# Kernel tuning notes

Hardware: AMD Instinct MI355X
Metric: run time of the kernel (lower is better)

## Reference

```python
import jax, jax.numpy as jnp
import numpy as np

N_NODES = 500000
N_EDGES = 5000000
D = 16


def _glorot(key, shape):
    fan_in, fan_out = shape[1], shape[0]
    lim = (6.0 / (fan_in + fan_out)) ** 0.5
    return jax.random.uniform(key, shape, jnp.float32, -lim, lim)


def setup_inputs() -> dict:
    key = jax.random.key(0)
    ks = jax.random.split(key, 12)
    x = jax.random.normal(ks[0], (N_NODES, D), jnp.float32)
    edge_index = jax.random.randint(ks[1], (2, N_EDGES), 0, N_NODES, jnp.int32)
    # GraphConv params: lin_rel (weight+bias, applied to aggregated neighbors),
    # lin_root (weight only, applied to self features)
    conv1_w_rel = _glorot(ks[2], (D, D))
    conv1_b_rel = jnp.zeros((D,), jnp.float32)
    conv1_w_root = _glorot(ks[3], (D, D))
    conv2_w_rel = _glorot(ks[4], (D, D))
    conv2_b_rel = jnp.zeros((D,), jnp.float32)
    conv2_w_root = _glorot(ks[5], (D, D))
    fc1_w = _glorot(ks[6], (8, D))
    fc1_b = jnp.zeros((8,), jnp.float32)
    fc2_w = _glorot(ks[7], (2, 8))
    fc2_b = jnp.zeros((2,), jnp.float32)
    return {
        "x": x, "edge_index": edge_index,
        "conv1_w_rel": conv1_w_rel, "conv1_b_rel": conv1_b_rel, "conv1_w_root": conv1_w_root,
        "conv2_w_rel": conv2_w_rel, "conv2_b_rel": conv2_b_rel, "conv2_w_root": conv2_w_root,
        "fc1_w": fc1_w, "fc1_b": fc1_b, "fc2_w": fc2_w, "fc2_b": fc2_b,
    }


def graph_conv(x, edge_index, w_rel, b_rel, w_root):
    # PyG GraphConv (aggr='add'): out_i = W_rel @ sum_{j->i} x_j + b_rel + W_root @ x_i
    src, dst = edge_index[0], edge_index[1]
    msgs = x[src]  # [E, D] gather of source-node features
    agg = jax.ops.segment_sum(msgs, dst, num_segments=x.shape[0])  # [N, D]
    return agg @ w_rel.T + b_rel + x @ w_root.T


def reference(x, edge_index,
              conv1_w_rel, conv1_b_rel, conv1_w_root,
              conv2_w_rel, conv2_b_rel, conv2_w_root,
              fc1_w, fc1_b, fc2_w, fc2_b):
    h = jax.nn.relu(graph_conv(x, edge_index, conv1_w_rel, conv1_b_rel, conv1_w_root))
    h = jax.nn.relu(graph_conv(h, edge_index, conv2_w_rel, conv2_b_rel, conv2_w_root))
    h = jax.nn.relu(h @ fc1_w.T + fc1_b)
    return h @ fc2_w.T + fc2_b
```

## Files before the change

kernel.cpp:

```cpp
#include <hip/hip_runtime.h>

#define N_NODES 500000
#define N_EDGES 5000000
#define D 16

__global__ __launch_bounds__(256) void scatter_add_kernel(
    const float* __restrict__ feat,
    const int* __restrict__ edge_index,
    float* __restrict__ agg) {
    long tid = (long)blockIdx.x * blockDim.x + threadIdx.x;
    long total = (long)N_EDGES * D;
    if (tid >= total) return;
    int e = (int)(tid >> 4);
    int d = (int)(tid & 15);
    int s = edge_index[e];
    int t = edge_index[N_EDGES + e];
    float v = feat[(long)s * D + d];
    atomicAdd(&agg[(long)t * D + d], v);
}

__global__ __launch_bounds__(256) void node1_kernel(
    const float* __restrict__ x,
    const float* __restrict__ agg,
    const float* __restrict__ w_rel,
    const float* __restrict__ b_rel,
    const float* __restrict__ w_root,
    float* __restrict__ h) {
    __shared__ float sWrel[D * D];
    __shared__ float sWroot[D * D];
    __shared__ float sB[D];
    for (int i = threadIdx.x; i < D * D; i += blockDim.x) {
        sWrel[i] = w_rel[i];
        sWroot[i] = w_root[i];
    }
    if (threadIdx.x < D) sB[threadIdx.x] = b_rel[threadIdx.x];
    __syncthreads();

    int i = blockIdx.x * blockDim.x + threadIdx.x;
    if (i >= N_NODES) return;

    float a[D], xi[D];
    {
        const float4* ap = (const float4*)(agg + (long)i * D);
        const float4* xp = (const float4*)(x + (long)i * D);
        #pragma unroll
        for (int q = 0; q < 4; ++q) {
            float4 av = ap[q];
            float4 xv = xp[q];
            a[q * 4 + 0] = av.x; a[q * 4 + 1] = av.y; a[q * 4 + 2] = av.z; a[q * 4 + 3] = av.w;
            xi[q * 4 + 0] = xv.x; xi[q * 4 + 1] = xv.y; xi[q * 4 + 2] = xv.z; xi[q * 4 + 3] = xv.w;
        }
    }

    float4* hp = (float4*)(h + (long)i * D);
    #pragma unroll
    for (int q = 0; q < 4; ++q) {
        float4 o;
        float* op = &o.x;
        #pragma unroll
        for (int r = 0; r < 4; ++r) {
            int dd = q * 4 + r;
            float acc = sB[dd];
            #pragma unroll
            for (int k = 0; k < D; ++k)
                acc += a[k] * sWrel[dd * D + k] + xi[k] * sWroot[dd * D + k];
            op[r] = acc > 0.f ? acc : 0.f;
        }
        hp[q] = o;
    }
}

__global__ __launch_bounds__(256) void node2_kernel(
    const float* __restrict__ h1,
    const float* __restrict__ agg,
    const float* __restrict__ w_rel,
    const float* __restrict__ b_rel,
    const float* __restrict__ w_root,
    const float* __restrict__ fc1_w,
    const float* __restrict__ fc1_b,
    const float* __restrict__ fc2_w,
    const float* __restrict__ fc2_b,
    float* __restrict__ out) {
    __shared__ float sWrel[D * D];
    __shared__ float sWroot[D * D];
    __shared__ float sB[D];
    __shared__ float sF1w[8 * D];
    __shared__ float sF1b[8];
    __shared__ float sF2w[2 * 8];
    __shared__ float sF2b[2];
    for (int i = threadIdx.x; i < D * D; i += blockDim.x) {
        sWrel[i] = w_rel[i];
        sWroot[i] = w_root[i];
    }
    if (threadIdx.x < D) sB[threadIdx.x] = b_rel[threadIdx.x];
    if (threadIdx.x < 8 * D) sF1w[threadIdx.x] = fc1_w[threadIdx.x];
    if (threadIdx.x < 8) sF1b[threadIdx.x] = fc1_b[threadIdx.x];
    if (threadIdx.x < 16) sF2w[threadIdx.x] = fc2_w[threadIdx.x];
    if (threadIdx.x < 2) sF2b[threadIdx.x] = fc2_b[threadIdx.x];
    __syncthreads();

    int i = blockIdx.x * blockDim.x + threadIdx.x;
    if (i >= N_NODES) return;

    float a[D], xi[D];
    {
        const float4* ap = (const float4*)(agg + (long)i * D);
        const float4* xp = (const float4*)(h1 + (long)i * D);
        #pragma unroll
        for (int q = 0; q < 4; ++q) {
            float4 av = ap[q];
            float4 xv = xp[q];
            a[q * 4 + 0] = av.x; a[q * 4 + 1] = av.y; a[q * 4 + 2] = av.z; a[q * 4 + 3] = av.w;
            xi[q * 4 + 0] = xv.x; xi[q * 4 + 1] = xv.y; xi[q * 4 + 2] = xv.z; xi[q * 4 + 3] = xv.w;
        }
    }

    float h2[D];
    #pragma unroll
    for (int dd = 0; dd < D; ++dd) {
        float acc = sB[dd];
        #pragma unroll
        for (int k = 0; k < D; ++k)
            acc += a[k] * sWrel[dd * D + k] + xi[k] * sWroot[dd * D + k];
        h2[dd] = acc > 0.f ? acc : 0.f;
    }

    float h3[8];
    #pragma unroll
    for (int j = 0; j < 8; ++j) {
        float acc = sF1b[j];
        #pragma unroll
        for (int k = 0; k < D; ++k) acc += h2[k] * sF1w[j * D + k];
        h3[j] = acc > 0.f ? acc : 0.f;
    }

    float2 o;
    {
        float acc0 = sF2b[0], acc1 = sF2b[1];
        #pragma unroll
        for (int j = 0; j < 8; ++j) {
            acc0 += h3[j] * sF2w[0 * 8 + j];
            acc1 += h3[j] * sF2w[1 * 8 + j];
        }
        o.x = acc0;
        o.y = acc1;
    }
    ((float2*)out)[i] = o;
}

extern "C" void kernel_launch(void* const* d_in, const int* in_sizes, int n_in,
                              void* d_out, int out_size, void* d_ws, size_t ws_size,
                              hipStream_t stream) {
    const float* x          = (const float*)d_in[0];
    const int*   edge_index = (const int*)d_in[1];
    const float* c1_wrel    = (const float*)d_in[2];
    const float* c1_brel    = (const float*)d_in[3];
    const float* c1_wroot   = (const float*)d_in[4];
    const float* c2_wrel    = (const float*)d_in[5];
    const float* c2_brel    = (const float*)d_in[6];
    const float* c2_wroot   = (const float*)d_in[7];
    const float* fc1_w      = (const float*)d_in[8];
    const float* fc1_b      = (const float*)d_in[9];
    const float* fc2_w      = (const float*)d_in[10];
    const float* fc2_b      = (const float*)d_in[11];
    float* out = (float*)d_out;

    float* agg = (float*)d_ws;
    float* h1  = agg + (long)N_NODES * D;
    size_t feat_bytes = (size_t)N_NODES * D * sizeof(float);

    const int BLK = 256;
    long scatter_total = (long)N_EDGES * D;
    int scatter_blocks = (int)((scatter_total + BLK - 1) / BLK);
    int node_blocks = (N_NODES + BLK - 1) / BLK;

    hipMemsetAsync(agg, 0, feat_bytes, stream);
    scatter_add_kernel<<<scatter_blocks, BLK, 0, stream>>>(x, edge_index, agg);
    node1_kernel<<<node_blocks, BLK, 0, stream>>>(x, agg, c1_wrel, c1_brel, c1_wroot, h1);

    hipMemsetAsync(agg, 0, feat_bytes, stream);
    scatter_add_kernel<<<scatter_blocks, BLK, 0, stream>>>(h1, edge_index, agg);
    node2_kernel<<<node_blocks, BLK, 0, stream>>>(h1, agg, c2_wrel, c2_brel, c2_wroot,
                                                  fc1_w, fc1_b, fc2_w, fc2_b, out);
}
```

Before: 702.6 us.

## Build CSR by destination and replace atomic scatter with pull-based gather

Builds a CSR keyed by destination node on every call: degree histogram, a three-kernel prefix scan, then an atomic-cursor reorder of source indices. Both conv layers then pull neighbour features per node with 16 threads per node and fuse aggregation with the node linear layers, removing the 80M float atomics and the agg buffers with their memsets. The price is CSR construction each call, which costs 10M integer atomics plus extra launches, and per-node loops whose length depends on degree.

```diff
diff --git a/kernel.cpp b/kernel.cpp
--- a/kernel.cpp
+++ b/kernel.cpp
@@ -4,148 +4,196 @@
 #define N_EDGES 5000000
 #define D 16
 
-__global__ __launch_bounds__(256) void scatter_add_kernel(
-    const float* __restrict__ feat,
-    const int* __restrict__ edge_index,
-    float* __restrict__ agg) {
-    long tid = (long)blockIdx.x * blockDim.x + threadIdx.x;
-    long total = (long)N_EDGES * D;
-    if (tid >= total) return;
-    int e = (int)(tid >> 4);
-    int d = (int)(tid & 15);
+#define SCAN_CHUNK 1024
+#define NSCAN_BLOCKS ((N_NODES + SCAN_CHUNK - 1) / SCAN_CHUNK)
+
+__global__ __launch_bounds__(256) void hist_kernel(
+    const int* __restrict__ edge_index, int* __restrict__ deg) {
+    int e = blockIdx.x * 256 + threadIdx.x;
+    if (e < N_EDGES) atomicAdd(&deg[edge_index[N_EDGES + e]], 1);
+}
+
+__global__ __launch_bounds__(256) void scan_blocks_kernel(
+    const int* __restrict__ deg, int* __restrict__ scanned,
+    int* __restrict__ partials) {
+    __shared__ int sdata[256];
+    int t = threadIdx.x;
+    int base = blockIdx.x * SCAN_CHUNK + t * 4;
+    int v0 = 0, v1 = 0, v2 = 0, v3 = 0;
+    if (base + 0 < N_NODES) v0 = deg[base + 0];
+    if (base + 1 < N_NODES) v1 = deg[base + 1];
+    if (base + 2 < N_NODES) v2 = deg[base + 2];
+    if (base + 3 < N_NODES) v3 = deg[base + 3];
+    int tsum = v0 + v1 + v2 + v3;
+    sdata[t] = tsum;
+    __syncthreads();
+    for (int off = 1; off < 256; off <<= 1) {
+        int val = (t >= off) ? sdata[t - off] : 0;
+        __syncthreads();
+        if (t >= off) sdata[t] += val;
+        __syncthreads();
+    }
+    int excl = sdata[t] - tsum;
+    if (t == 255) partials[blockIdx.x] = sdata[255];
+    int p = excl;
+    if (base + 0 < N_NODES) scanned[base + 0] = p; p += v0;
+    if (base + 1 < N_NODES) scanned[base + 1] = p; p += v1;
+    if (base + 2 < N_NODES) scanned[base + 2] = p; p += v2;
+    if (base + 3 < N_NODES) scanned[base + 3] = p;
+}
+
+__global__ __launch_bounds__(512) void scan_partials_kernel(int* __restrict__ partials) {
+    __shared__ int sdata[512];
+    int t = threadIdx.x;
+    int v = (t < NSCAN_BLOCKS) ? partials[t] : 0;
+    sdata[t] = v;
+    __syncthreads();
+    for (int off = 1; off < 512; off <<= 1) {
+        int val = (t >= off) ? sdata[t - off] : 0;
+        __syncthreads();
+        if (t >= off) sdata[t] += val;
+        __syncthreads();
+    }
+    if (t < NSCAN_BLOCKS) partials[t] = sdata[t] - v;
+}
+
+__global__ __launch_bounds__(256) void scan_add_kernel(
+    const int* __restrict__ scanned, const int* __restrict__ partials,
+    int* __restrict__ rowptr, int* __restrict__ cursor) {
+    int i = blockIdx.x * 256 + threadIdx.x;
+    if (i < N_NODES) {
+        int v = scanned[i] + partials[i / SCAN_CHUNK];
+        rowptr[i] = v;
+        cursor[i] = v;
+    }
+    if (i == 0) rowptr[N_NODES] = N_EDGES;
+}
+
+__global__ __launch_bounds__(256) void reorder_kernel(
+    const int* __restrict__ edge_index, int* __restrict__ cursor,
+    int* __restrict__ csr_src) {
+    int e = blockIdx.x * 256 + threadIdx.x;
+    if (e >= N_EDGES) return;
     int s = edge_index[e];
     int t = edge_index[N_EDGES + e];
-    float v = feat[(long)s * D + d];
-    atomicAdd(&agg[(long)t * D + d], v);
-}
-
-__global__ __launch_bounds__(256) void node1_kernel(
+    int pos = atomicAdd(&cursor[t], 1);
+    csr_src[pos] = s;
+}
+
+__global__ __launch_bounds__(256) void gather_node1_kernel(
     const float* __restrict__ x,
-    const float* __restrict__ agg,
-    const float* __restrict__ w_rel,
-    const float* __restrict__ b_rel,
+    const int* __restrict__ rowptr, const int* __restrict__ csr_src,
+    const float* __restrict__ w_rel, const float* __restrict__ b_rel,
+    const float* __restrict__ w_root, float* __restrict__ h) {
+    __shared__ float sWrelT[D * D];
+    __shared__ float sWrootT[D * D];
+    __shared__ float sB[D];
+    __shared__ float sAgg[16][D + 1];
+    __shared__ float sX[16][D + 1];
+
+    {
+        int r = threadIdx.x >> 4, c = threadIdx.x & 15;
+        sWrelT[c * D + r] = w_rel[r * D + c];
+        sWrootT[c * D + r] = w_root[r * D + c];
+        if (threadIdx.x < D) sB[threadIdx.x] = b_rel[threadIdx.x];
+    }
+    __syncthreads();
+
+    int g = threadIdx.x >> 4;
+    int d = threadIdx.x & 15;
+    int node = blockIdx.x * 16 + g;
+
+    if (node < N_NODES) {
+        int r0 = rowptr[node], r1 = rowptr[node + 1];
+        float acc = 0.f;
+        for (int j = r0; j < r1; ++j) {
+            int s = csr_src[j];
+            acc += x[(long)s * D + d];
+        }
+        sAgg[g][d] = acc;
+        sX[g][d] = x[(long)node * D + d];
+    }
+    __syncthreads();
+
+    if (node < N_NODES) {
+        float accO = sB[d];
+        #pragma unroll
+        for (int k = 0; k < D; ++k)
+            accO += sAgg[g][k] * sWrelT[k * D + d] + sX[g][k] * sWrootT[k * D + d];
+        h[(long)node * D + d] = accO > 0.f ? accO : 0.f;
+    }
+}
+
+__global__ __launch_bounds__(256) void gather_node2_kernel(
+    const float* __restrict__ h1,
+    const int* __restrict__ rowptr, const int* __restrict__ csr_src,
+    const float* __restrict__ w_rel, const float* __restrict__ b_rel,
     const float* __restrict__ w_root,
-    float* __restrict__ h) {
-    __shared__ float sWrel[D * D];
-    __shared__ float sWroot[D * D];
-    __shared__ float sB[D];
-    for (int i = threadIdx.x; i < D * D; i += blockDim.x) {
-        sWrel[i] = w_rel[i];
-        sWroot[i] = w_root[i];
-    }
-    if (threadIdx.x < D) sB[threadIdx.x] = b_rel[threadIdx.x];
-    __syncthreads();
-
-    int i = blockIdx.x * blockDim.x + threadIdx.x;
-    if (i >= N_NODES) return;
-
-    float a[D], xi[D];
-    {
-        const float4* ap = (const float4*)(agg + (long)i * D);
-        const float4* xp = (const float4*)(x + (long)i * D);
-        #pragma unroll
-        for (int q = 0; q < 4; ++q) {
-            float4 av = ap[q];
-            float4 xv = xp[q];
-            a[q * 4 + 0] = av.x; a[q * 4 + 1] = av.y; a[q * 4 + 2] = av.z; a[q * 4 + 3] = av.w;
-            xi[q * 4 + 0] = xv.x; xi[q * 4 + 1] = xv.y; xi[q * 4 + 2] = xv.z; xi[q * 4 + 3] = xv.w;
-        }
-    }
-
-    float4* hp = (float4*)(h + (long)i * D);
-    #pragma unroll
-    for (int q = 0; q < 4; ++q) {
-        float4 o;
-        float* op = &o.x;
-        #pragma unroll
-        for (int r = 0; r < 4; ++r) {
-            int dd = q * 4 + r;
-            float acc = sB[dd];
-            #pragma unroll
-            for (int k = 0; k < D; ++k)
-                acc += a[k] * sWrel[dd * D + k] + xi[k] * sWroot[dd * D + k];
-            op[r] = acc > 0.f ? acc : 0.f;
-        }
-        hp[q] = o;
-    }
-}
-
-__global__ __launch_bounds__(256) void node2_kernel(
-    const float* __restrict__ h1,
-    const float* __restrict__ agg,
-    const float* __restrict__ w_rel,
-    const float* __restrict__ b_rel,
-    const float* __restrict__ w_root,
-    const float* __restrict__ fc1_w,
-    const float* __restrict__ fc1_b,
-    const float* __restrict__ fc2_w,
-    const float* __restrict__ fc2_b,
+    const float* __restrict__ fc1_w, const float* __restrict__ fc1_b,
+    const float* __restrict__ fc2_w, const float* __restrict__ fc2_b,
     float* __restrict__ out) {
-    __shared__ float sWrel[D * D];
-    __shared__ float sWroot[D * D];
+    __shared__ float sWrelT[D * D];
+    __shared__ float sWrootT[D * D];
     __shared__ float sB[D];
     __shared__ float sF1w[8 * D];
     __shared__ float sF1b[8];
     __shared__ float sF2w[2 * 8];
     __shared__ float sF2b[2];
-    for (int i = threadIdx.x; i < D * D; i += blockDim.x) {
-        sWrel[i] = w_rel[i];
-        sWroot[i] = w_root[i];
-    }
-    if (threadIdx.x < D) sB[threadIdx.x] = b_rel[threadIdx.x];
-    if (threadIdx.x < 8 * D) sF1w[threadIdx.x] = fc1_w[threadIdx.x];
-    if (threadIdx.x < 8) sF1b[threadIdx.x] = fc1_b[threadIdx.x];
-    if (threadIdx.x < 16) sF2w[threadIdx.x] = fc2_w[threadIdx.x];
-    if (threadIdx.x < 2) sF2b[threadIdx.x] = fc2_b[threadIdx.x];
-    __syncthreads();
-
-    int i = blockIdx.x * blockDim.x + threadIdx.x;
-    if (i >= N_NODES) return;
-
-    float a[D], xi[D];
+    __shared__ float sAgg[16][D + 1];
+    __shared__ float sX[16][D + 1];
+    __shared__ float sH2[16][D + 1];
+
     {
-        const float4* ap = (const float4*)(agg + (long)i * D);
-        const float4* xp = (const float4*)(h1 + (long)i * D);
-        #pragma unroll
-        for (int q = 0; q < 4; ++q) {
-            float4 av = ap[q];
-            float4 xv = xp[q];
-            a[q * 4 + 0] = av.x; a[q * 4 + 1] = av.y; a[q * 4 + 2] = av.z; a[q * 4 + 3] = av.w;
-            xi[q * 4 + 0] = xv.x; xi[q * 4 + 1] = xv.y; xi[q * 4 + 2] = xv.z; xi[q * 4 + 3] = xv.w;
+        int r = threadIdx.x >> 4, c = threadIdx.x & 15;
+        sWrelT[c * D + r] = w_rel[r * D + c];
+        sWrootT[c * D + r] = w_root[r * D + c];
+        if (threadIdx.x < D) sB[threadIdx.x] = b_rel[threadIdx.x];
+        if (threadIdx.x < 8 * D) sF1w[threadIdx.x] = fc1_w[threadIdx.x];
+        if (threadIdx.x < 8) sF1b[threadIdx.x] = fc1_b[threadIdx.x];
+        if (threadIdx.x < 16) sF2w[threadIdx.x] = fc2_w[threadIdx.x];
+        if (threadIdx.x < 2) sF2b[threadIdx.x] = fc2_b[threadIdx.x];
+    }
+    __syncthreads();
+
+    int g = threadIdx.x >> 4;
+    int d = threadIdx.x & 15;
+    int node = blockIdx.x * 16 + g;
+
+    if (node < N_NODES) {
+        int r0 = rowptr[node], r1 = rowptr[node + 1];
+        float acc = 0.f;
+        for (int j = r0; j < r1; ++j) {
+            int s = csr_src[j];
+            acc += h1[(long)s * D + d];
         }
-    }
-
-    float h2[D];
-    #pragma unroll
-    for (int dd = 0; dd < D; ++dd) {
-        float acc = sB[dd];
+        sAgg[g][d] = acc;
+        sX[g][d] = h1[(long)node * D + d];
+    }
+    __syncthreads();
+
+    if (node < N_NODES) {
+        float accO = sB[d];
         #pragma unroll
         for (int k = 0; k < D; ++k)
-            acc += a[k] * sWrel[dd * D + k] + xi[k] * sWroot[dd * D + k];
-        h2[dd] = acc > 0.f ? acc : 0.f;
-    }
-
-    float h3[8];
-    #pragma unroll
-    for (int j = 0; j < 8; ++j) {
-        float acc = sF1b[j];
-        #pragma unroll
-        for (int k = 0; k < D; ++k) acc += h2[k] * sF1w[j * D + k];
-        h3[j] = acc > 0.f ? acc : 0.f;
-    }
-
-    float2 o;
-    {
-        float acc0 = sF2b[0], acc1 = sF2b[1];
+            accO += sAgg[g][k] * sWrelT[k * D + d] + sX[g][k] * sWrootT[k * D + d];
+        sH2[g][d] = accO > 0.f ? accO : 0.f;
+    }
+    __syncthreads();
+
+    if (node < N_NODES && d < 2) {
+        float h3[8];
         #pragma unroll
         for (int j = 0; j < 8; ++j) {
-            acc0 += h3[j] * sF2w[0 * 8 + j];
-            acc1 += h3[j] * sF2w[1 * 8 + j];
+            float acc = sF1b[j];
+            #pragma unroll
+            for (int k = 0; k < D; ++k) acc += sH2[g][k] * sF1w[j * D + k];
+            h3[j] = acc > 0.f ? acc : 0.f;
         }
-        o.x = acc0;
-        o.y = acc1;
-    }
-    ((float2*)out)[i] = o;
+        float o = sF2b[d];
+        #pragma unroll
+        for (int j = 0; j < 8; ++j) o += h3[j] * sF2w[d * 8 + j];
+        out[(long)node * 2 + d] = o;
+    }
 }
 
 extern "C" void kernel_launch(void* const* d_in, const int* in_sizes, int n_in,
@@ -165,21 +213,30 @@
     const float* fc2_b      = (const float*)d_in[11];
     float* out = (float*)d_out;
 
-    float* agg = (float*)d_ws;
-    float* h1  = agg + (long)N_NODES * D;
-    size_t feat_bytes = (size_t)N_NODES * D * sizeof(float);
+    int* csr_src  = (int*)d_ws;
+    int* rowptr   = csr_src + N_EDGES;
+    int* cursor   = rowptr + (N_NODES + 1);
+    int* deg      = cursor + N_NODES;
+    int* scanned  = deg + N_NODES;
+    int* partials = scanned + N_NODES;
+    float* h1     = (float*)(partials + 512);
 
     const int BLK = 256;
-    long scatter_total = (long)N_EDGES * D;
-    int scatter_blocks = (int)((scatter_total + BLK - 1) / BLK);
-    int node_blocks = (N_NODES + BLK - 1) / BLK;
-
-    hipMemsetAsync(agg, 0, feat_bytes, stream);
-    scatter_add_kernel<<<scatter_blocks, BLK, 0, stream>>>(x, edge_index, agg);
-    node1_kernel<<<node_blocks, BLK, 0, stream>>>(x, agg, c1_wrel, c1_brel, c1_wroot, h1);
-
-    hipMemsetAsync(agg, 0, feat_bytes, stream);
-    scatter_add_kernel<<<scatter_blocks, BLK, 0, stream>>>(h1, edge_index, agg);
-    node2_kernel<<<node_blocks, BLK, 0, stream>>>(h1, agg, c2_wrel, c2_brel, c2_wroot,
-                                                  fc1_w, fc1_b, fc2_w, fc2_b, out);
-}
+    int edge_blocks = (N_EDGES + BLK - 1) / BLK;
+    int node_blocks16 = (N_NODES + 15) / 16;
+    int node_blocks256 = (N_NODES + BLK - 1) / BLK;
+
+    hipMemsetAsync(deg, 0, N_NODES * sizeof(int), stream);
+    hist_kernel<<<edge_blocks, BLK, 0, stream>>>(edge_index, deg);
+    scan_blocks_kernel<<<NSCAN_BLOCKS, BLK, 0, stream>>>(deg, scanned, partials);
+    scan_partials_kernel<<<1, 512, 0, stream>>>(partials);
+    scan_add_kernel<<<node_blocks256, BLK, 0, stream>>>(scanned, partials, rowptr, cursor);
+    reorder_kernel<<<edge_blocks, BLK, 0, stream>>>(edge_index, cursor, csr_src);
+
+    gather_node1_kernel<<<node_blocks16, BLK, 0, stream>>>(
+        x, rowptr, csr_src, c1_wrel, c1_brel, c1_wroot, h1);
+
+    gather_node2_kernel<<<node_blocks16, BLK, 0, stream>>>(
+        h1, rowptr, csr_src, c2_wrel, c2_brel, c2_wroot,
+        fc1_w, fc1_b, fc2_w, fc2_b, out);
+}
```

Measured after the change: 1.321 ms. 1.88x slower.

## Store aggregation and hidden features in fp16 with packed half2 atomics

Applied to the files above, without the earlier changes.

The aggregation buffer and the intermediate layer-1 features move from fp32 to packed half2. Each thread now handles two features, using one packed fp16 atomic add per pair, so the count of atomics and the bytes moved in the scatter-add halve. The node kernels convert between fp16 and fp32 at load and store time. The cost is reduced precision in summed neighbour aggregates, with rounding error in the accumulation and possible overflow for high-degree nodes.

```diff
diff --git a/kernel.cpp b/kernel.cpp
--- a/kernel.cpp
+++ b/kernel.cpp
@@ -1,31 +1,45 @@
 #include <hip/hip_runtime.h>
+#include <hip/hip_fp16.h>
 
 #define N_NODES 500000
 #define N_EDGES 5000000
 #define D 16
 
-__global__ __launch_bounds__(256) void scatter_add_kernel(
-    const float* __restrict__ feat,
+__global__ __launch_bounds__(256) void scatter1_kernel(
+    const float* __restrict__ x,
     const int* __restrict__ edge_index,
-    float* __restrict__ agg) {
-    long tid = (long)blockIdx.x * blockDim.x + threadIdx.x;
-    long total = (long)N_EDGES * D;
-    if (tid >= total) return;
-    int e = (int)(tid >> 4);
-    int d = (int)(tid & 15);
+    __half2* __restrict__ agg) {
+    long tid = (long)blockIdx.x * 256 + threadIdx.x;
+    if (tid >= (long)N_EDGES * 8) return;
+    int e = (int)(tid >> 3);
+    int p = (int)(tid & 7);
     int s = edge_index[e];
     int t = edge_index[N_EDGES + e];
-    float v = feat[(long)s * D + d];
-    atomicAdd(&agg[(long)t * D + d], v);
+    float2 v = ((const float2*)(x + (long)s * D))[p];
+    unsafeAtomicAdd(&agg[(long)t * 8 + p], __float22half2_rn(v));
+}
+
+__global__ __launch_bounds__(256) void scatter2_kernel(
+    const __half2* __restrict__ h1,
+    const int* __restrict__ edge_index,
+    __half2* __restrict__ agg) {
+    long tid = (long)blockIdx.x * 256 + threadIdx.x;
+    if (tid >= (long)N_EDGES * 8) return;
+    int e = (int)(tid >> 3);
+    int p = (int)(tid & 7);
+    int s = edge_index[e];
+    int t = edge_index[N_EDGES + e];
+    __half2 v = h1[(long)s * 8 + p];
+    unsafeAtomicAdd(&agg[(long)t * 8 + p], v);
 }
 
 __global__ __launch_bounds__(256) void node1_kernel(
     const float* __restrict__ x,
-    const float* __restrict__ agg,
+    const __half2* __restrict__ agg,
     const float* __restrict__ w_rel,
     const float* __restrict__ b_rel,
     const float* __restrict__ w_root,
-    float* __restrict__ h) {
+    __half2* __restrict__ h1) {
     __shared__ float sWrel[D * D];
     __shared__ float sWroot[D * D];
     __shared__ float sB[D];
@@ -41,38 +55,48 @@
 
     float a[D], xi[D];
     {
-        const float4* ap = (const float4*)(agg + (long)i * D);
+        __half2 hrow[8];
+        const float4* ap = (const float4*)(agg + (long)i * 8);
+        *(float4*)&hrow[0] = ap[0];
+        *(float4*)&hrow[4] = ap[1];
+        #pragma unroll
+        for (int q = 0; q < 8; ++q) {
+            float2 f = __half22float2(hrow[q]);
+            a[2 * q] = f.x; a[2 * q + 1] = f.y;
+        }
         const float4* xp = (const float4*)(x + (long)i * D);
         #pragma unroll
         for (int q = 0; q < 4; ++q) {
-            float4 av = ap[q];
             float4 xv = xp[q];
-            a[q * 4 + 0] = av.x; a[q * 4 + 1] = av.y; a[q * 4 + 2] = av.z; a[q * 4 + 3] = av.w;
-            xi[q * 4 + 0] = xv.x; xi[q * 4 + 1] = xv.y; xi[q * 4 + 2] = xv.z; xi[q * 4 + 3] = xv.w;
-        }
-    }
-
-    float4* hp = (float4*)(h + (long)i * D);
+            xi[q * 4 + 0] = xv.x; xi[q * 4 + 1] = xv.y;
+            xi[q * 4 + 2] = xv.z; xi[q * 4 + 3] = xv.w;
+        }
+    }
+
+    __half2 hout[8];
     #pragma unroll
-    for (int q = 0; q < 4; ++q) {
-        float4 o;
-        float* op = &o.x;
-        #pragma unroll
-        for (int r = 0; r < 4; ++r) {
-            int dd = q * 4 + r;
+    for (int q = 0; q < 8; ++q) {
+        float o0, o1;
+        #pragma unroll
+        for (int r = 0; r < 2; ++r) {
+            int dd = 2 * q + r;
             float acc = sB[dd];
             #pragma unroll
             for (int k = 0; k < D; ++k)
                 acc += a[k] * sWrel[dd * D + k] + xi[k] * sWroot[dd * D + k];
-            op[r] = acc > 0.f ? acc : 0.f;
-        }
-        hp[q] = o;
-    }
+            acc = acc > 0.f ? acc : 0.f;
+            if (r == 0) o0 = acc; else o1 = acc;
+        }
+        hout[q] = __float22half2_rn(make_float2(o0, o1));
+    }
+    float4* hp = (float4*)(h1 + (long)i * 8);
+    hp[0] = *(float4*)&hout[0];
+    hp[1] = *(float4*)&hout[4];
 }
 
 __global__ __launch_bounds__(256) void node2_kernel(
-    const float* __restrict__ h1,
-    const float* __restrict__ agg,
+    const __half2* __restrict__ h1,
+    const __half2* __restrict__ agg,
     const float* __restrict__ w_rel,
     const float* __restrict__ b_rel,
     const float* __restrict__ w_root,
@@ -104,14 +128,22 @@
 
     float a[D], xi[D];
     {
-        const float4* ap = (const float4*)(agg + (long)i * D);
-        const float4* xp = (const float4*)(h1 + (long)i * D);
-        #pragma unroll
-        for (int q = 0; q < 4; ++q) {
-            float4 av = ap[q];
-            float4 xv = xp[q];
-            a[q * 4 + 0] = av.x; a[q * 4 + 1] = av.y; a[q * 4 + 2] = av.z; a[q * 4 + 3] = av.w;
-            xi[q * 4 + 0] = xv.x; xi[q * 4 + 1] = xv.y; xi[q * 4 + 2] = xv.z; xi[q * 4 + 3] = xv.w;
+        __half2 hrow[8];
+        const float4* ap = (const float4*)(agg + (long)i * 8);
+        *(float4*)&hrow[0] = ap[0];
+        *(float4*)&hrow[4] = ap[1];
+        #pragma unroll
+        for (int q = 0; q < 8; ++q) {
+            float2 f = __half22float2(hrow[q]);
+            a[2 * q] = f.x; a[2 * q + 1] = f.y;
+        }
+        const float4* xp = (const float4*)(h1 + (long)i * 8);
+        *(float4*)&hrow[0] = xp[0];
+        *(float4*)&hrow[4] = xp[1];
+        #pragma unroll
+        for (int q = 0; q < 8; ++q) {
+            float2 f = __half22float2(hrow[q]);
+            xi[2 * q] = f.x; xi[2 * q + 1] = f.y;
         }
     }
 
@@ -165,21 +197,21 @@
     const float* fc2_b      = (const float*)d_in[11];
     float* out = (float*)d_out;
 
-    float* agg = (float*)d_ws;
-    float* h1  = agg + (long)N_NODES * D;
-    size_t feat_bytes = (size_t)N_NODES * D * sizeof(float);
+    __half2* agg = (__half2*)d_ws;
+    __half2* h1  = agg + (long)N_NODES * 8;
+    size_t agg_bytes = (size_t)N_NODES * 8 * sizeof(__half2);
 
     const int BLK = 256;
-    long scatter_total = (long)N_EDGES * D;
+    long scatter_total = (long)N_EDGES * 8;
     int scatter_blocks = (int)((scatter_total + BLK - 1) / BLK);
     int node_blocks = (N_NODES + BLK - 1) / BLK;
 
-    hipMemsetAsync(agg, 0, feat_bytes, stream);
-    scatter_add_kernel<<<scatter_blocks, BLK, 0, stream>>>(x, edge_index, agg);
+    hipMemsetAsync(agg, 0, agg_bytes, stream);
+    scatter1_kernel<<<scatter_blocks, BLK, 0, stream>>>(x, edge_index, agg);
     node1_kernel<<<node_blocks, BLK, 0, stream>>>(x, agg, c1_wrel, c1_brel, c1_wroot, h1);
 
-    hipMemsetAsync(agg, 0, feat_bytes, stream);
-    scatter_add_kernel<<<scatter_blocks, BLK, 0, stream>>>(h1, edge_index, agg);
+    hipMemsetAsync(agg, 0, agg_bytes, stream);
+    scatter2_kernel<<<scatter_blocks, BLK, 0, stream>>>(h1, edge_index, agg);
     node2_kernel<<<node_blocks, BLK, 0, stream>>>(h1, agg, c2_wrel, c2_brel, c2_wroot,
                                                   fc1_w, fc1_b, fc2_w, fc2_b, out);
 }
```

New measurement: 661.0 us. -5.9%, faster.
